# Kernel tuning notes

Measured on AMD Instinct MI355X. Metric: run time of the kernel, lower is better.

Reference implementation:

```python
import jax, jax.numpy as jnp
import numpy as np

B, S, C, HEADS, EXP = 8, 1024, 256, 8, 4
H = W = 32  # S = H*W
HID = EXP * C
RATES = (1, 6, 12, 18)
EPS = 1e-5


def _conv(x, w, b=None, dilation=1, padding=0):
    out = jax.lax.conv_general_dilated(
        x, w, (1, 1), [(padding, padding), (padding, padding)],
        rhs_dilation=(dilation, dilation),
        dimension_numbers=('NCHW', 'OIHW', 'NCHW'))
    if b is not None:
        out = out + b[None, :, None, None]
    return out


def _bn(x, g, b, m, v):
    # inference-mode BatchNorm2d
    s = (g / jnp.sqrt(v + EPS))[None, :, None, None]
    return (x - m[None, :, None, None]) * s + b[None, :, None, None]


def _ln(x, g, b):
    mu = jnp.mean(x, -1, keepdims=True)
    var = jnp.mean((x - mu) ** 2, -1, keepdims=True)
    return (x - mu) / jnp.sqrt(var + EPS) * g + b


def setup_inputs() -> dict:
    key = jax.random.key(0)
    ks = iter(jax.random.split(key, 64))

    def n(shape, s=0.05):
        return jax.random.normal(next(ks), shape, jnp.float32) * s

    def u(shape):
        return jax.random.uniform(next(ks), shape, jnp.float32, 0.5, 1.5)

    inp = {
        'value': n((B, S, C), 1.0),
        'key': n((B, S, C), 1.0),
        'query': n((B, S, C), 1.0),
        'res': n((B, S, C), 1.0),
        # nn.MultiheadAttention params
        'attn_wi': n((3 * C, C)), 'attn_bi': jnp.zeros((3 * C,)),
        'attn_wo': n((C, C)), 'attn_bo': jnp.zeros((C,)),
        # Modulator params
        'mod_bias': jnp.zeros((1, C, 1, 1)),
        'ca_w1': n((C // 16, C)), 'ca_w2': n((C, C // 16)),
        'pa_w': n((C, C, 1, 1)),
        'pa_bn_g': jnp.ones((C,)), 'pa_bn_b': jnp.zeros((C,)),
        'pa_bn_m': n((C,), 0.1), 'pa_bn_v': u((C,)),
        'sa_w': n((4, C, C, 3, 3)), 'sa_b': jnp.zeros((4, C)),
        'sa_bn_g': jnp.ones((4, C)), 'sa_bn_b': jnp.zeros((4, C)),
        'sa_bn_m': n((4, C), 0.1), 'sa_bn_v': u((4, C)),
        'sa_out_w': n((C, 4 * C, 1, 1)), 'sa_out_b': jnp.zeros((C,)),
        'out_w': n((C, C, 1, 1)), 'out_b': jnp.zeros((C,)),
        'out_bn_g': jnp.ones((C,)), 'out_bn_b': jnp.zeros((C,)),
        'out_bn_m': n((C,), 0.1), 'out_bn_v': u((C,)),
        # LayerNorms
        'ln1_g': jnp.ones((C,)), 'ln1_b': jnp.zeros((C,)),
        'ln2_g': jnp.ones((C,)), 'ln2_b': jnp.zeros((C,)),
        # E_MLP params
        'mlp_w1': n((HID, C)), 'mlp_b1': jnp.zeros((HID,)),
        'dw_w': n((HID, HID, 3, 3), 0.02), 'dw_b': jnp.zeros((HID,)),
        'pw_w': n((HID, HID, 3, 3), 0.02), 'pw_b': jnp.zeros((HID,)),
        'mlp_w2': n((C, HID)), 'mlp_b2': jnp.zeros((C,)),
    }
    return inp


def reference(value, key, query, res,
              attn_wi, attn_bi, attn_wo, attn_bo,
              mod_bias, ca_w1, ca_w2, pa_w,
              pa_bn_g, pa_bn_b, pa_bn_m, pa_bn_v,
              sa_w, sa_b, sa_bn_g, sa_bn_b, sa_bn_m, sa_bn_v,
              sa_out_w, sa_out_b, out_w, out_b,
              out_bn_g, out_bn_b, out_bn_m, out_bn_v,
              ln1_g, ln1_b, ln2_g, ln2_b,
              mlp_w1, mlp_b1, dw_w, dw_b, pw_w, pw_b, mlp_w2, mlp_b2):
    d = C // HEADS
    # SMA arg shuffle: block calls sma(query,key,value) -> SMA(value=query,key=key,query=value)
    # -> nn.MultiheadAttention(query=value_blk, key=key_blk, value=query_blk)
    q = (value @ attn_wi[:C].T + attn_bi[:C]).reshape(B, S, HEADS, d)
    k = (key @ attn_wi[C:2 * C].T + attn_bi[C:2 * C]).reshape(B, S, HEADS, d)
    v = (query @ attn_wi[2 * C:].T + attn_bi[2 * C:]).reshape(B, S, HEADS, d)
    scores = jnp.einsum('bqhd,bkhd->bhqk', q, k) / jnp.sqrt(jnp.float32(d))
    attn = jax.nn.softmax(scores, axis=-1)
    ctx = jnp.einsum('bhqk,bkhd->bqhd', attn, v).reshape(B, S, C)
    msa = ctx @ attn_wo.T + attn_bo                       # [B,S,C]

    x = msa.transpose(0, 2, 1).reshape(B, C, H, W)        # [B,C,H,W]

    # --- Modulator ---
    pa = x * jax.nn.sigmoid(_bn(_conv(x, pa_w), pa_bn_g, pa_bn_b, pa_bn_m, pa_bn_v))
    y = jnp.mean(x, axis=(2, 3))                          # [B,C]
    y = jax.nn.sigmoid(jax.nn.relu(y @ ca_w1.T) @ ca_w2.T)
    ca = x * y[:, :, None, None]
    pa_ca = jax.nn.softmax(pa @ ca, axis=-1)              # [B,C,H,H] (H==W)
    sa_outs = [_bn(jax.nn.relu(_conv(x, sa_w[i], sa_b[i], dilation=r, padding=r)),
                   sa_bn_g[i], sa_bn_b[i], sa_bn_m[i], sa_bn_v[i])
               for i, r in enumerate(RATES)]
    sa = _conv(jnp.concatenate(sa_outs, axis=1), sa_out_w, sa_out_b)
    out = pa_ca @ sa                                      # [B,C,H,W]
    out = _bn(_conv(out, out_w, out_b), out_bn_g, out_bn_b, out_bn_m, out_bn_v)
    syn = out + mod_bias + x                              # residual inside modulator

    attn_seq = syn.reshape(B, C, S).transpose(0, 2, 1)    # [B,S,C]
    q2 = _ln(attn_seq + res, ln1_g, ln1_b)

    # --- E_MLP ---
    h = jax.nn.gelu(q2 @ mlp_w1.T + mlp_b1, approximate=False)  # [B,S,4C]
    hc = h.transpose(0, 2, 1).reshape(B, HID, H, W)
    hc = _conv(hc, dw_w, dw_b, padding=1)
    hc = _conv(hc, pw_w, pw_b, padding=1)
    h2 = hc.reshape(B, HID, S).transpose(0, 2, 1)
    ff = h2 @ mlp_w2.T + mlp_b2
    return _ln(ff + q2, ln2_g, ln2_b)
```

## Files before the change

### kernel.cpp

```cpp
#include <hip/hip_runtime.h>
#include <hip/hip_bf16.h>
#include <math.h>

typedef __attribute__((ext_vector_type(8))) short bf16x8;
typedef __attribute__((ext_vector_type(4))) short bf16x4;
typedef __attribute__((ext_vector_type(4))) float f32x4;

#define MM 8192
#define CC 256

__device__ __forceinline__ short f2bf(float f) {
  unsigned u = __float_as_uint(f);
  u = (u + 0x7FFFu + ((u >> 16) & 1u)) >> 16;
  return (short)u;
}

__device__ __forceinline__ void gload16(const short* g, short* l) {
  __builtin_amdgcn_global_load_lds(
      (const __attribute__((address_space(1))) unsigned int*)(g),
      (__attribute__((address_space(3))) unsigned int*)(l), 16, 0, 0);
}

__global__ __launch_bounds__(256, 2) void convh_k(const short* __restrict__ Ain,
                                                  const short* __restrict__ Wt,
                                                  short* __restrict__ outB,
                                                  const float* __restrict__ bias) {
  extern __shared__ short sm[];
  const int tid = threadIdx.x;
  const int bx = blockIdx.x;
  const int bm = bx & 63, bn = bx >> 6;
  const int l = tid & 63, w = tid >> 6;
  const int wm = w >> 1, wn = w & 1;
  const int lr = l & 15, lg = l >> 4;
  const int lsub = l >> 3;
  const int srcu = (l & 7) ^ lsub;
  const int img = bm >> 3, rbase = (bm & 7) * 4;
  const bf16x8 zv = {0, 0, 0, 0, 0, 0, 0, 0};

  f32x4 acc[4][4];
#pragma unroll
  for (int i = 0; i < 4; ++i)
#pragma unroll
    for (int j = 0; j < 4; ++j) acc[i][j] = (f32x4){0.f, 0.f, 0.f, 0.f};

  const short* wsrc[4];
#pragma unroll
  for (int i = 0; i < 4; ++i) {
    int rowi = (w * 4 + i) * 8 + lsub;
    wsrc[i] = Wt + (size_t)(bn * 128 + rowi) * 1024 + srcu * 8;
  }

  const short* asrc[6]; int apos[6]; bool avalid[6];
#pragma unroll
  for (int i = 0; i < 6; ++i) {
    int ug = tid + i * 256;
    int pos = ug >> 3, u = ug & 7;
    int irow = pos >> 5, px = pos & 31;
    int grow = rbase + irow - 1;
    avalid[i] = ((unsigned)grow < 32u);
    int growc = grow < 0 ? 0 : (grow > 31 ? 31 : grow);
    asrc[i] = Ain + ((size_t)(img * 1024 + growc * 32 + px)) * 1024 + u * 8;
    apos[i] = pos * 64 + ((u ^ (pos & 7)) << 3);
  }

  bf16x8 areg[6];
  auto issueA = [&](int kc) {
#pragma unroll
    for (int i = 0; i < 6; ++i)
      areg[i] = *(const bf16x8*)(asrc[i] + kc * 64);
  };
  auto writeA = [&](int ab) {
    short* abuf = sm + 16384 + ab * 12288;
#pragma unroll
    for (int i = 0; i < 6; ++i)
      *(bf16x8*)(abuf + apos[i]) = avalid[i] ? areg[i] : zv;
  };
  auto issueW = [&](int kc, int tap, int wb) {
    short* base = sm + wb * 8192;
    size_t wo = (size_t)tap * 1048576 + (size_t)kc * 64;
#pragma unroll
    for (int i = 0; i < 4; ++i)
      gload16(wsrc[i] + wo, base + (w * 4 + i) * 512);
  };
  auto compute = [&](int dy, int dx, const short* bA, const short* bB) {
    __builtin_amdgcn_s_setprio(1);
#pragma unroll
    for (int ks = 0; ks < 64; ks += 32) {
      const int u = (ks >> 3) + lg;
      bf16x8 af[4], bfr[4];
#pragma unroll
      for (int mt = 0; mt < 4; ++mt) {
        int px = (mt & 1) * 16 + lr;
        int ipx = px + dx;
        bool okx = ((unsigned)ipx < 32u);
        int pos = (wm * 2 + (mt >> 1) + 1 + dy) * 32 + (ipx & 31);
        bf16x8 v = *(const bf16x8*)&bA[pos * 64 + ((u ^ (pos & 7)) << 3)];
        af[mt] = okx ? v : zv;
      }
#pragma unroll
      for (int nt = 0; nt < 4; ++nt)
        bfr[nt] = *(const bf16x8*)&bB[(wn * 64 + nt * 16 + lr) * 64 + ((u ^ (lr & 7)) << 3)];
#pragma unroll
      for (int mt = 0; mt < 4; ++mt)
#pragma unroll
        for (int nt = 0; nt < 4; ++nt)
          acc[mt][nt] = __builtin_amdgcn_mfma_f32_16x16x32_bf16(af[mt], bfr[nt], acc[mt][nt], 0, 0, 0);
    }
    __builtin_amdgcn_s_setprio(0);
  };

  issueA(0);
  issueW(0, 0, 0);
  issueW(0, 1, 1);
  asm volatile("s_waitcnt vmcnt(4)" ::: "memory");
  writeA(0);
  asm volatile("s_waitcnt lgkmcnt(0)" ::: "memory");

  for (int kc = 0; kc < 16; ++kc) {
    const int ab = kc & 1;
    const short* bA = sm + 16384 + ab * 12288;
#pragma unroll
    for (int tap = 0; tap < 9; ++tap) {
      const int wb = (kc + tap) & 1;
      const short* bB = sm + wb * 8192;
      if (tap == 7) {
        if (kc < 15) asm volatile("s_waitcnt vmcnt(10)" ::: "memory");
        else         asm volatile("s_waitcnt vmcnt(4)" ::: "memory");
      } else if (tap == 8) {
        if (kc < 15) asm volatile("s_waitcnt vmcnt(4)" ::: "memory");
        else         asm volatile("s_waitcnt vmcnt(0)" ::: "memory");
      } else {
        asm volatile("s_waitcnt vmcnt(4)" ::: "memory");
      }
      asm volatile("s_barrier" ::: "memory");
      compute(tap / 3 - 1, tap % 3 - 1, bA, bB);
      asm volatile("s_barrier" ::: "memory");
      if (tap <= 6) {
        if (tap == 6 && kc < 15) issueA(kc + 1);
        issueW(kc, tap + 2, wb);
      } else if (tap == 7) {
        if (kc < 15) issueW(kc + 1, 0, wb);
      } else {
        if (kc < 15) {
          writeA(ab ^ 1);
          asm volatile("s_waitcnt lgkmcnt(0)" ::: "memory");
          issueW(kc + 1, 1, wb);
        }
      }
    }
  }

#pragma unroll
  for (int nt = 0; nt < 4; ++nt) {
    const int col = bn * 128 + wn * 64 + nt * 16 + lr;
    const float bi = bias[col];
#pragma unroll
    for (int mt = 0; mt < 4; ++mt) {
      const int row0 = bm * 128 + wm * 64 + mt * 16 + lg * 4;
#pragma unroll
      for (int j = 0; j < 4; ++j)
        outB[(size_t)(row0 + j) * 1024 + col] = f2bf(acc[mt][nt][j] + bi);
    }
  }
}

struct GP {
  const short* A; const short* W; float* outF; short* outB; float* outT;
  const float* bias; const float* scale; const float* shift; const float* aux;
  const short* zero;
  long aZStride, wZStride, oZStride;
  int N, Kc, ldA, ldOut, outColOff, outZOff;
  int dil0, dil1, dil2, dil3;
  int T, nkcs;
};

template<int TAPS, int EPI, int OUTMODE, int TSTORE>
__global__ __launch_bounds__(256, 2) void gemmd_k(GP p) {
  extern __shared__ short sm[];
  const int tid = threadIdx.x;
  const int bx = blockIdx.x, bz = blockIdx.z;
  const int bm = bx & 63, bn = bx >> 6;
  const int l = tid & 63, w = tid >> 6;
  const int wm = w >> 1, wn = w & 1;
  const int lr = l & 15, lg = l >> 4;
  const int lsub = l >> 3;
  const int srcu = (l & 7) ^ lsub;

  const short* Abase = p.A + (size_t)bz * p.aZStride;
  const short* Wbase = p.W + (size_t)bz * p.wZStride;
  const int dil = (TAPS == 9)
      ? (bz == 0 ? p.dil0 : bz == 1 ? p.dil1 : bz == 2 ? p.dil2 : p.dil3) : 1;

  f32x4 acc[4][4];
#pragma unroll
  for (int i = 0; i < 4; ++i)
#pragma unroll
    for (int j = 0; j < 4; ++j) acc[i][j] = (f32x4){0.f, 0.f, 0.f, 0.f};

  int rowi[4], prow[4], bimg[4], py[4], px[4];
  const short* wsrc[4];
#pragma unroll
  for (int i = 0; i < 4; ++i) {
    rowi[i] = (w * 4 + i) * 8 + lsub;
    prow[i] = bm * 128 + rowi[i];
    bimg[i] = prow[i] >> 10; py[i] = (prow[i] >> 5) & 31; px[i] = prow[i] & 31;
    wsrc[i] = Wbase + (size_t)(bn * 128 + rowi[i]) * p.Kc + srcu * 8;
  }
  const size_t wTap = (size_t)p.N * p.Kc;
  const int nkcMask = (1 << p.nkcs) - 1;

  auto issue = [&](int t, int buf) {
    const int tap = t >> p.nkcs;
    const int kc = t & nkcMask;
    short* base = sm + buf * 16384;
    if (TAPS == 1) {
#pragma unroll
      for (int i = 0; i < 4; ++i)
        gload16(Abase + (size_t)prow[i] * p.ldA + kc * 64 + srcu * 8,
                base + (w * 4 + i) * 512);
    } else {
      const int dy = (tap / 3 - 1) * dil, dx = (tap % 3 - 1) * dil;
#pragma unroll
      for (int i = 0; i < 4; ++i) {
        int yy = py[i] + dy, xx = px[i] + dx;
        bool ok = ((unsigned)yy < 32u) & ((unsigned)xx < 32u);
        const short* a = ok
            ? Abase + (size_t)((bimg[i] << 10) + (yy << 5) + xx) * p.ldA + kc * 64
            : p.zero;
        gload16(a + srcu * 8, base + (w * 4 + i) * 512);
      }
    }
    short* bbase = base + 8192;
    const size_t wo = (size_t)tap * wTap + kc * 64;
#pragma unroll
    for (int i = 0; i < 4; ++i)
      gload16(wsrc[i] + wo, bbase + (w * 4 + i) * 512);
  };

  auto compute = [&](int buf) {
    const short* bA = sm + buf * 16384;
    const short* bB = bA + 8192;
    __builtin_amdgcn_s_setprio(1);
#pragma unroll
    for (int ks = 0; ks < 64; ks += 32) {
      const int u = (ks >> 3) + lg;
      bf16x8 af[4], bfr[4];
#pragma unroll
      for (int mt = 0; mt < 4; ++mt)
        af[mt] = *(bf16x8*)&bA[(wm * 64 + mt * 16 + lr) * 64 + ((u ^ (lr & 7)) << 3)];
#pragma unroll
      for (int nt = 0; nt < 4; ++nt)
        bfr[nt] = *(bf16x8*)&bB[(wn * 64 + nt * 16 + lr) * 64 + ((u ^ (lr & 7)) << 3)];
#pragma unroll
      for (int mt = 0; mt < 4; ++mt)
#pragma unroll
        for (int nt = 0; nt < 4; ++nt)
          acc[mt][nt] = __builtin_amdgcn_mfma_f32_16x16x32_bf16(af[mt], bfr[nt], acc[mt][nt], 0, 0, 0);
    }
    __builtin_amdgcn_s_setprio(0);
  };

  issue(0, 0);
  if (p.T > 1) issue(1, 1);
  int cur = 0;
  for (int t = 0; t < p.T; ++t) {
    if (t + 1 < p.T) asm volatile("s_waitcnt vmcnt(8)" ::: "memory");
    else             asm volatile("s_waitcnt vmcnt(0)" ::: "memory");
    asm volatile("s_barrier" ::: "memory");
    compute(cur);
    asm volatile("s_barrier" ::: "memory");
    if (t + 2 < p.T) issue(t + 2, cur);
    cur ^= 1;
  }

  float* outF = p.outF + (size_t)bz * p.oZStride;
  short* outB = p.outB + (size_t)bz * p.oZStride;
#pragma unroll
  for (int nt = 0; nt < 4; ++nt) {
    const int col = bn * 128 + wn * 64 + nt * 16 + lr;
    const int gcol = p.outColOff + bz * p.outZOff + col;
    const float bi = (p.bias != nullptr) ? p.bias[bz * p.N + col] : 0.f;
    float scl = 0.f, shf = 0.f;
    if (EPI == 3 || EPI == 4 || EPI == 5) {
      scl = p.scale[bz * p.N + col]; shf = p.shift[bz * p.N + col];
    }
#pragma unroll
    for (int mt = 0; mt < 4; ++mt) {
      const int row0 = bm * 128 + wm * 64 + mt * 16 + lg * 4;
      f32x4 vv;
#pragma unroll
      for (int j = 0; j < 4; ++j) {
        const long row = row0 + j;
        float v = acc[mt][nt][j];
        if (EPI == 1 || EPI == 2 || EPI == 3) v += bi;
        if (EPI == 2) v = 0.5f * v * (1.f + erff(v * 0.70710678118654752f));
        if (EPI == 3) { v = fmaxf(v, 0.f); v = v * scl + shf; }
        if (EPI == 4) {
          float t2 = v * scl + shf;
          float sg = 1.f / (1.f + __expf(-t2));
          v = p.aux[row * 256 + col] * sg;
        }
        if (EPI == 5) v = v * scl + shf + p.aux[row * 256 + col];
        vv[j] = v;
        if (OUTMODE == 0 || OUTMODE == 2) outF[row * (long)p.ldOut + gcol] = v;
        if (OUTMODE == 1 || OUTMODE == 2) outB[row * (long)p.ldOut + gcol] = f2bf(v);
      }
      if (TSTORE) {
        float* t = p.outT + ((size_t)(row0 >> 10) * 256 + gcol) * 1024 + (row0 & 1023);
        *(f32x4*)t = vv;
      }
    }
  }
}

__global__ __launch_bounds__(256) void attn_k(const short* qb, const short* kb,
                                              const short* vb, short* ctx) {
  __shared__ short lK[128 * 40];
  __shared__ short lVt[32 * 136];
  __shared__ short lP[4][16 * 136];
  const int tid = threadIdx.x;
  const int qt = blockIdx.x;
  const int bh = blockIdx.y;
  const int b = bh >> 3, h = bh & 7;
  const int l = tid & 63, wv = tid >> 6;
  const int lr = l & 15, lg = l >> 4;
  const float SC = 0.17677669529663687f;

  const int qrow = qt * 64 + wv * 16 + lr;
  const bf16x8 qf = *(const bf16x8*)(qb + ((size_t)(b * 1024 + qrow)) * 256 + h * 32 + lg * 8);

  f32x4 o0 = {0.f,0.f,0.f,0.f}, o1 = {0.f,0.f,0.f,0.f};
  float m[4] = {-1e30f, -1e30f, -1e30f, -1e30f};
  float lsum[4] = {0.f, 0.f, 0.f, 0.f};

  for (int ch = 0; ch < 8; ++ch) {
    __syncthreads();
    {
      const int keyi = tid >> 1, d0 = (tid & 1) * 16;
      const short* src = kb + ((size_t)(b * 1024 + ch * 128 + keyi)) * 256 + h * 32 + d0;
      short* dst = &lK[keyi * 40 + d0];
      *(bf16x8*)dst = *(const bf16x8*)src;
      *(bf16x8*)(dst + 8) = *(const bf16x8*)(src + 8);
    }
    {
      const int keyi = tid >> 1, d0 = (tid & 1) * 16;
      const short* src = vb + ((size_t)(b * 1024 + ch * 128 + keyi)) * 256 + h * 32 + d0;
      short tmp[16];
      *(bf16x8*)tmp = *(const bf16x8*)src;
      *(bf16x8*)(tmp + 8) = *(const bf16x8*)(src + 8);
#pragma unroll
      for (int j = 0; j < 16; ++j) lVt[(d0 + j) * 136 + keyi] = tmp[j];
    }
    __syncthreads();

    f32x4 sc[8];
#pragma unroll
    for (int jt = 0; jt < 8; ++jt) {
      bf16x8 bfr = *(bf16x8*)&lK[(jt * 16 + lr) * 40 + lg * 8];
      sc[jt] = __builtin_amdgcn_mfma_f32_16x16x32_bf16(qf, bfr, (f32x4){0.f,0.f,0.f,0.f}, 0, 0, 0);
      sc[jt] *= SC;
    }
#pragma unroll
    for (int j = 0; j < 4; ++j) {
      float rm = -1e30f;
#pragma unroll
      for (int jt = 0; jt < 8; ++jt) rm = fmaxf(rm, sc[jt][j]);
      rm = fmaxf(rm, __shfl_xor(rm, 1));
      rm = fmaxf(rm, __shfl_xor(rm, 2));
      rm = fmaxf(rm, __shfl_xor(rm, 4));
      rm = fmaxf(rm, __shfl_xor(rm, 8));
      float mn = fmaxf(m[j], rm);
      float alpha = exp2f((m[j] - mn) * 1.44269504088896f);
      m[j] = mn;
      float rs = 0.f;
#pragma unroll
      for (int jt = 0; jt < 8; ++jt) {
        float pv = exp2f((sc[jt][j] - mn) * 1.44269504088896f);
        sc[jt][j] = pv;
        rs += pv;
      }
      rs += __shfl_xor(rs, 1); rs += __shfl_xor(rs, 2);
      rs += __shfl_xor(rs, 4); rs += __shfl_xor(rs, 8);
      lsum[j] = lsum[j] * alpha + rs;
      o0[j] *= alpha; o1[j] *= alpha;
      const int prw = lg * 4 + j;
#pragma unroll
      for (int jt = 0; jt < 8; ++jt) lP[wv][prw * 136 + jt * 16 + lr] = f2bf(sc[jt][j]);
    }
#pragma unroll
    for (int kc = 0; kc < 4; ++kc) {
      bf16x8 pf = *(bf16x8*)&lP[wv][lr * 136 + kc * 32 + lg * 8];
      bf16x8 v0 = *(bf16x8*)&lVt[lr * 136 + kc * 32 + lg * 8];
      bf16x8 v1 = *(bf16x8*)&lVt[(16 + lr) * 136 + kc * 32 + lg * 8];
      o0 = __builtin_amdgcn_mfma_f32_16x16x32_bf16(pf, v0, o0, 0, 0, 0);
      o1 = __builtin_amdgcn_mfma_f32_16x16x32_bf16(pf, v1, o1, 0, 0, 0);
    }
  }
  const size_t orow = (size_t)(b * 1024 + qt * 64 + wv * 16);
#pragma unroll
  for (int j = 0; j < 4; ++j) {
    float inv = 1.f / lsum[j];
    ctx[(orow + lg * 4 + j) * 256 + h * 32 + lr]      = f2bf(o0[j] * inv);
    ctx[(orow + lg * 4 + j) * 256 + h * 32 + 16 + lr] = f2bf(o1[j] * inv);
  }
}

__global__ __launch_bounds__(256) void cvt4_k(const float* src, short* dst, int n4) {
  int i = blockIdx.x * 256 + threadIdx.x;
  if (i < n4) {
    f32x4 v = ((const f32x4*)src)[i];
    bf16x4 o;
    o[0] = f2bf(v[0]); o[1] = f2bf(v[1]); o[2] = f2bf(v[2]); o[3] = f2bf(v[3]);
    ((bf16x4*)dst)[i] = o;
  }
}

__global__ __launch_bounds__(256) void zero_k(short* p) {
  p[blockIdx.x * 256 + threadIdx.x] = 0;
}

__global__ __launch_bounds__(256) void tap_k(const float* src, short* dst, int n) {
  int i = blockIdx.x * 256 + threadIdx.x;
  if (i >= n) return;
  const float* s = src + (size_t)i * 9;
  float v[9];
#pragma unroll
  for (int t = 0; t < 9; ++t) v[t] = s[t];
#pragma unroll
  for (int t = 0; t < 9; ++t) dst[(size_t)t * n + i] = f2bf(v[t]);
}

__global__ void bnprep_k(const float* pg, const float* pb, const float* pm, const float* pv,
                         const float* sg, const float* sb, const float* sm, const float* sv,
                         const float* og, const float* ob, const float* om, const float* ov,
                         const float* conv_ob, const float* mbias, float* out) {
  int c = threadIdx.x;
  float s = pg[c] / sqrtf(pv[c] + 1e-5f);
  out[c] = s;
  out[256 + c] = pb[c] - pm[c] * s;
  for (int i = 0; i < 4; ++i) {
    int idx = i * 256 + c;
    float ss = sg[idx] / sqrtf(sv[idx] + 1e-5f);
    out[512 + idx] = ss;
    out[1536 + idx] = sb[idx] - sm[idx] * ss;
  }
  float os = og[c] / sqrtf(ov[c] + 1e-5f);
  out[2560 + c] = os;
  out[2816 + c] = ob[c] - om[c] * os + conv_ob[c] * os + mbias[c];
}

__global__ __launch_bounds__(256) void tposeb_k(const float* src, short* dst) {
  __shared__ float tile[32][33];
  int pc = blockIdx.x, cc = blockIdx.y, b = blockIdx.z;
  int tx = threadIdx.x & 31, ty = threadIdx.x >> 5;
  const float* s = src + ((size_t)b * 256 + cc * 32) * 1024 + pc * 32;
#pragma unroll
  for (int k = 0; k < 4; ++k)
    tile[ty + 8 * k][tx] = s[(ty + 8 * k) * 1024 + tx];
  __syncthreads();
  short* d = dst + ((size_t)b * 1024 + pc * 32) * 256 + cc * 32;
#pragma unroll
  for (int k = 0; k < 4; ++k)
    d[(ty + 8 * k) * 256 + tx] = f2bf(tile[tx][ty + 8 * k]);
}

__global__ __launch_bounds__(256) void camean_k(const float* x, float* partial) {
  int blk = blockIdx.x, c = threadIdx.x;
  const float* px = x + ((size_t)blk * 64) * 256 + c;
  float s = 0.f;
#pragma unroll 4
  for (int r = 0; r < 64; ++r) s += px[(size_t)r * 256];
  partial[blk * 256 + c] = s;
}

__global__ __launch_bounds__(256) void ca2_k(const float* partial, const float* w1,
                                             const float* w2, float* y2) {
  __shared__ float ly[256];
  __shared__ float ly1[16];
  int b = blockIdx.x, c = threadIdx.x;
  float s = 0.f;
#pragma unroll
  for (int j = 0; j < 16; ++j) s += partial[(b * 16 + j) * 256 + c];
  ly[c] = s * (1.f / 1024.f);
  __syncthreads();
  if (c < 16) {
    float a = 0.f;
    const float* wp = w1 + c * 256;
    for (int i = 0; i < 256; ++i) a += ly[i] * wp[i];
    ly1[c] = fmaxf(a, 0.f);
  }
  __syncthreads();
  float a = 0.f;
  const float* wp = w2 + c * 16;
#pragma unroll
  for (int j = 0; j < 16; ++j) a += ly1[j] * wp[j];
  y2[b * 256 + c] = 1.f / (1.f + __expf(-a));
}

__global__ __launch_bounds__(256) void bm1_k(const float* paT, const float* xT,
                                             const float* y2, float* pa_ca) {
  __shared__ float sp[32][33], sx[32][33], so[32][33];
  __shared__ float rinv[32];
  int bc = blockIdx.x, t = threadIdx.x;
  for (int e = t; e < 1024; e += 256) {
    sp[e >> 5][e & 31] = paT[(size_t)bc * 1024 + e];
    sx[e >> 5][e & 31] = xT[(size_t)bc * 1024 + e];
  }
  __syncthreads();
  float yv = y2[bc];
  int i = t >> 3, j0 = (t & 7) * 4;
  float a0 = 0.f, a1 = 0.f, a2 = 0.f, a3 = 0.f;
  for (int k = 0; k < 32; ++k) {
    float pv = sp[i][k];
    a0 += pv * sx[k][j0];     a1 += pv * sx[k][j0 + 1];
    a2 += pv * sx[k][j0 + 2]; a3 += pv * sx[k][j0 + 3];
  }
  so[i][j0] = a0 * yv; so[i][j0 + 1] = a1 * yv;
  so[i][j0 + 2] = a2 * yv; so[i][j0 + 3] = a3 * yv;
  __syncthreads();
  if (t < 32) {
    float mx = -1e30f;
    for (int j = 0; j < 32; ++j) mx = fmaxf(mx, so[t][j]);
    float sum = 0.f;
    for (int j = 0; j < 32; ++j) { float pp = __expf(so[t][j] - mx); so[t][j] = pp; sum += pp; }
    rinv[t] = 1.f / sum;
  }
  __syncthreads();
  for (int e = t; e < 1024; e += 256)
    pa_ca[(size_t)bc * 1024 + e] = so[e >> 5][e & 31] * rinv[e >> 5];
}

__global__ __launch_bounds__(256) void bm2_k(const float* pa_ca, const float* saT, float* moT) {
  __shared__ float sp[32][33], ss[32][33];
  int bc = blockIdx.x, t = threadIdx.x;
  for (int e = t; e < 1024; e += 256) {
    sp[e >> 5][e & 31] = pa_ca[(size_t)bc * 1024 + e];
    ss[e >> 5][e & 31] = saT[(size_t)bc * 1024 + e];
  }
  __syncthreads();
  int i = t >> 3, j0 = (t & 7) * 4;
  float a0 = 0.f, a1 = 0.f, a2 = 0.f, a3 = 0.f;
  for (int k = 0; k < 32; ++k) {
    float pv = sp[i][k];
    a0 += pv * ss[k][j0];     a1 += pv * ss[k][j0 + 1];
    a2 += pv * ss[k][j0 + 2]; a3 += pv * ss[k][j0 + 3];
  }
  size_t base = (size_t)bc * 1024 + i * 32 + j0;
  moT[base] = a0; moT[base + 1] = a1; moT[base + 2] = a2; moT[base + 3] = a3;
}

template<int DUAL>
__global__ __launch_bounds__(256) void ln_k(const float* in, const float* res,
                                            const float* g, const float* bta,
                                            float* out, short* outB) {
  __shared__ float red[8];
  size_t row = blockIdx.x;
  int c = threadIdx.x;
  int wv = c >> 6, lane = c & 63;
  float v = in[row * 256 + c] + res[row * 256 + c];
  float s = v;
  for (int mk = 1; mk < 64; mk <<= 1) s += __shfl_xor(s, mk);
  if (lane == 0) red[wv] = s;
  __syncthreads();
  float mu = (red[0] + red[1] + red[2] + red[3]) * (1.f / 256.f);
  float d = v - mu;
  float q = d * d;
  for (int mk = 1; mk < 64; mk <<= 1) q += __shfl_xor(q, mk);
  if (lane == 0) red[4 + wv] = q;
  __syncthreads();
  float var = (red[4] + red[5] + red[6] + red[7]) * (1.f / 256.f);
  float o = d * rsqrtf(var + 1e-5f) * g[c] + bta[c];
  out[row * 256 + c] = o;
  if (DUAL) outB[row * 256 + c] = f2bf(o);
}

extern "C" void kernel_launch(void* const* d_in, const int* in_sizes, int n_in,
                              void* d_out, int out_size, void* d_ws, size_t ws_size,
                              hipStream_t stream) {
  (void)in_sizes; (void)n_in; (void)out_size; (void)ws_size;
  const float* value    = (const float*)d_in[0];
  const float* key      = (const float*)d_in[1];
  const float* query    = (const float*)d_in[2];
  const float* res      = (const float*)d_in[3];
  const float* attn_wi  = (const float*)d_in[4];
  const float* attn_bi  = (const float*)d_in[5];
  const float* attn_wo  = (const float*)d_in[6];
  const float* attn_bo  = (const float*)d_in[7];
  const float* mod_bias = (const float*)d_in[8];
  const float* ca_w1    = (const float*)d_in[9];
  const float* ca_w2    = (const float*)d_in[10];
  const float* pa_w     = (const float*)d_in[11];
  const float* pa_bn_g  = (const float*)d_in[12];
  const float* pa_bn_b  = (const float*)d_in[13];
  const float* pa_bn_m  = (const float*)d_in[14];
  const float* pa_bn_v  = (const float*)d_in[15];
  const float* sa_w     = (const float*)d_in[16];
  const float* sa_b     = (const float*)d_in[17];
  const float* sa_bn_g  = (const float*)d_in[18];
  const float* sa_bn_b  = (const float*)d_in[19];
  const float* sa_bn_m  = (const float*)d_in[20];
  const float* sa_bn_v  = (const float*)d_in[21];
  const float* sa_out_w = (const float*)d_in[22];
  const float* sa_out_b = (const float*)d_in[23];
  const float* out_w    = (const float*)d_in[24];
  const float* out_b    = (const float*)d_in[25];
  const float* out_bn_g = (const float*)d_in[26];
  const float* out_bn_b = (const float*)d_in[27];
  const float* out_bn_m = (const float*)d_in[28];
  const float* out_bn_v = (const float*)d_in[29];
  const float* ln1_g    = (const float*)d_in[30];
  const float* ln1_b    = (const float*)d_in[31];
  const float* ln2_g    = (const float*)d_in[32];
  const float* ln2_b    = (const float*)d_in[33];
  const float* mlp_w1   = (const float*)d_in[34];
  const float* mlp_b1   = (const float*)d_in[35];
  const float* dw_w     = (const float*)d_in[36];
  const float* dw_b     = (const float*)d_in[37];
  const float* pw_w     = (const float*)d_in[38];
  const float* pw_b     = (const float*)d_in[39];
  const float* mlp_w2   = (const float*)d_in[40];
  const float* mlp_b2   = (const float*)d_in[41];

  char* ws = (char*)d_ws;
  const size_t MB = 1024 * 1024;
  char* A = ws + 0 * MB;
  char* Bx = ws + 16 * MB;
  char* Cx = ws + 32 * MB;
  float* xbuf  = (float*)(ws + 40 * MB);
  short* xbf   = (short*)(ws + 48 * MB);
  char* Fx = ws + 52 * MB;
  float* q2buf = (float*)(ws + 60 * MB);
  short* q2B   = (short*)(ws + 68 * MB);
  short* wdw   = (short*)(ws + 72 * MB);
  short* wpw   = (short*)(ws + 90 * MB);
  size_t o = 108 * MB;
  short* w_awi  = (short*)(ws + o); o += 768 * 256 * 2;
  short* w_awo  = (short*)(ws + o); o += 256 * 256 * 2;
  short* w_pa   = (short*)(ws + o); o += 256 * 256 * 2;
  short* w_sa   = (short*)(ws + o); o += (size_t)4 * 9 * 256 * 256 * 2;
  short* w_saou = (short*)(ws + o); o += 256 * 1024 * 2;
  short* w_out  = (short*)(ws + o); o += 256 * 256 * 2;
  short* w_mlp1 = (short*)(ws + o); o += 1024 * 256 * 2;
  short* w_mlp2 = (short*)(ws + o); o += 256 * 1024 * 2;
  float* bn     = (float*)(ws + o); o += 3072 * 4;
  float* y2buf  = (float*)(ws + o); o += 8 * 256 * 4;
  float* capart = (float*)(ws + o); o += 128 * 256 * 4;
  short* zbuf   = (short*)(ws + o); o += 2048 * 2;

  short* vkq  = (short*)A;
  short* qkv  = (short*)Bx;
  short* ctxB = (short*)Cx;
  float* xT   = (float*)A;
  float* paT  = (float*)(A + 8 * MB);
  float* pa_ca = (float*)Bx;
  short* saCat = (short*)A;
  float* saT  = (float*)Cx;
  float* moT  = (float*)Fx;
  short* modB = (short*)Cx;
  float* synBuf = (float*)Fx;
  short* hB   = (short*)A;
  short* hc1B = (short*)Bx;
  short* h2B  = (short*)A;
  float* ffBuf = (float*)Cx;

  const int LDSB = 2 * 16384 * 2;
  const int LDSC = 40960 * 2;
  hipFuncSetAttribute((const void*)gemmd_k<1, 1, 1, 0>, hipFuncAttributeMaxDynamicSharedMemorySize, LDSB);
  hipFuncSetAttribute((const void*)gemmd_k<1, 1, 2, 1>, hipFuncAttributeMaxDynamicSharedMemorySize, LDSB);
  hipFuncSetAttribute((const void*)gemmd_k<1, 4, 3, 1>, hipFuncAttributeMaxDynamicSharedMemorySize, LDSB);
  hipFuncSetAttribute((const void*)gemmd_k<9, 3, 1, 0>, hipFuncAttributeMaxDynamicSharedMemorySize, LDSB);
  hipFuncSetAttribute((const void*)gemmd_k<1, 1, 3, 1>, hipFuncAttributeMaxDynamicSharedMemorySize, LDSB);
  hipFuncSetAttribute((const void*)gemmd_k<1, 5, 0, 0>, hipFuncAttributeMaxDynamicSharedMemorySize, LDSB);
  hipFuncSetAttribute((const void*)gemmd_k<1, 2, 1, 0>, hipFuncAttributeMaxDynamicSharedMemorySize, LDSB);
  hipFuncSetAttribute((const void*)gemmd_k<1, 1, 0, 0>, hipFuncAttributeMaxDynamicSharedMemorySize, LDSB);
  hipFuncSetAttribute((const void*)convh_k, hipFuncAttributeMaxDynamicSharedMemorySize, LDSC);

  zero_k<<<8, 256, 0, stream>>>(zbuf);
  cvt4_k<<<192, 256, 0, stream>>>(attn_wi, w_awi, 768 * 64);
  cvt4_k<<<64, 256, 0, stream>>>(attn_wo, w_awo, 256 * 64);
  cvt4_k<<<64, 256, 0, stream>>>(pa_w, w_pa, 256 * 64);
  for (int i4 = 0; i4 < 4; ++i4)
    tap_k<<<256, 256, 0, stream>>>(sa_w + (size_t)i4 * 589824,
                                   w_sa + (size_t)i4 * 589824, 65536);
  cvt4_k<<<256, 256, 0, stream>>>(sa_out_w, w_saou, 1024 * 64);
  cvt4_k<<<64, 256, 0, stream>>>(out_w, w_out, 256 * 64);
  cvt4_k<<<256, 256, 0, stream>>>(mlp_w1, w_mlp1, 1024 * 64);
  cvt4_k<<<256, 256, 0, stream>>>(mlp_w2, w_mlp2, 1024 * 64);
  tap_k<<<4096, 256, 0, stream>>>(dw_w, wdw, 1048576);
  tap_k<<<4096, 256, 0, stream>>>(pw_w, wpw, 1048576);
  bnprep_k<<<1, 256, 0, stream>>>(pa_bn_g, pa_bn_b, pa_bn_m, pa_bn_v,
                                  sa_bn_g, sa_bn_b, sa_bn_m, sa_bn_v,
                                  out_bn_g, out_bn_b, out_bn_m, out_bn_v,
                                  out_b, mod_bias, bn);
  cvt4_k<<<2048, 256, 0, stream>>>(value, vkq, MM * 64);
  cvt4_k<<<2048, 256, 0, stream>>>(key,   vkq + (size_t)MM * 256, MM * 64);
  cvt4_k<<<2048, 256, 0, stream>>>(query, vkq + (size_t)2 * MM * 256, MM * 64);

  GP g;
  g.zero = zbuf; g.scale = nullptr; g.shift = nullptr; g.aux = nullptr;
  g.aZStride = 0; g.wZStride = 0; g.oZStride = 0;
  g.outColOff = 0; g.outZOff = 0;
  g.dil0 = 1; g.dil1 = 1; g.dil2 = 1; g.dil3 = 1;
  g.outF = nullptr; g.outB = nullptr; g.outT = nullptr;

  g.A = vkq; g.W = w_awi; g.outB = qkv; g.bias = attn_bi;
  g.N = 256; g.Kc = 256; g.ldA = 256; g.ldOut = 256; g.T = 4; g.nkcs = 2;
  g.aZStride = (size_t)MM * 256; g.wZStride = 256 * 256; g.oZStride = (size_t)MM * 256;
  gemmd_k<1, 1, 1, 0><<<dim3(128, 1, 3), 256, LDSB, stream>>>(g);
  g.aZStride = 0; g.wZStride = 0; g.oZStride = 0;

  attn_k<<<dim3(16, 64), 256, 0, stream>>>(qkv, qkv + (size_t)MM * 256,
                                           qkv + (size_t)2 * MM * 256, ctxB);

  g.A = ctxB; g.W = w_awo; g.outF = xbuf; g.outB = xbf; g.outT = xT; g.bias = attn_bo;
  gemmd_k<1, 1, 2, 1><<<dim3(128), 256, LDSB, stream>>>(g);

  g.A = xbf; g.W = w_pa; g.outF = nullptr; g.outB = nullptr; g.outT = paT; g.bias = nullptr;
  g.scale = bn; g.shift = bn + 256; g.aux = xbuf;
  gemmd_k<1, 4, 3, 1><<<dim3(128), 256, LDSB, stream>>>(g);
  g.scale = nullptr; g.shift = nullptr; g.aux = nullptr;

  camean_k<<<128, 256, 0, stream>>>(xbuf, capart);
  ca2_k<<<8, 256, 0, stream>>>(capart, ca_w1, ca_w2, y2buf);
  bm1_k<<<2048, 256, 0, stream>>>(paT, xT, y2buf, pa_ca);

  g.A = xbf; g.W = w_sa; g.outB = saCat; g.outF = nullptr; g.outT = nullptr;
  g.bias = sa_b; g.scale = bn + 512; g.shift = bn + 1536;
  g.ldOut = 1024; g.outZOff = 256; g.wZStride = (size_t)9 * 256 * 256;
  g.dil0 = 1; g.dil1 = 6; g.dil2 = 12; g.dil3 = 18;
  g.T = 36; g.nkcs = 2;
  gemmd_k<9, 3, 1, 0><<<dim3(128, 1, 4), 256, LDSB, stream>>>(g);
  g.outZOff = 0; g.wZStride = 0; g.scale = nullptr; g.shift = nullptr;
  g.dil0 = 1; g.dil1 = 1; g.dil2 = 1; g.dil3 = 1;

  g.A = saCat; g.W = w_saou; g.outB = nullptr; g.outT = saT; g.bias = sa_out_b;
  g.N = 256; g.Kc = 1024; g.ldA = 1024; g.ldOut = 256; g.T = 16; g.nkcs = 4;
  gemmd_k<1, 1, 3, 1><<<dim3(128), 256, LDSB, stream>>>(g);

  bm2_k<<<2048, 256, 0, stream>>>(pa_ca, saT, moT);
  tposeb_k<<<dim3(32, 8, 8), 256, 0, stream>>>(moT, modB);

  g.A = modB; g.W = w_out; g.outF = synBuf; g.outT = nullptr; g.bias = nullptr;
  g.scale = bn + 2560; g.shift = bn + 2816; g.aux = xbuf;
  g.N = 256; g.Kc = 256; g.ldA = 256; g.ldOut = 256; g.T = 4; g.nkcs = 2;
  gemmd_k<1, 5, 0, 0><<<dim3(128), 256, LDSB, stream>>>(g);
  g.scale = nullptr; g.shift = nullptr; g.aux = nullptr;

  ln_k<1><<<8192, 256, 0, stream>>>(synBuf, res, ln1_g, ln1_b, q2buf, q2B);

  g.A = q2B; g.W = w_mlp1; g.outB = hB; g.outF = nullptr; g.bias = mlp_b1;
  g.N = 1024; g.Kc = 256; g.ldA = 256; g.ldOut = 1024; g.T = 4; g.nkcs = 2;
  gemmd_k<1, 2, 1, 0><<<dim3(512), 256, LDSB, stream>>>(g);

  convh_k<<<dim3(512), 256, LDSC, stream>>>(hB, wdw, hc1B, dw_b);

  convh_k<<<dim3(512), 256, LDSC, stream>>>(hc1B, wpw, h2B, pw_b);

  g.A = h2B; g.W = w_mlp2; g.outF = ffBuf; g.outB = nullptr; g.bias = mlp_b2;
  g.N = 256; g.Kc = 1024; g.ldA = 1024; g.ldOut = 256; g.T = 16; g.nkcs = 4;
  gemmd_k<1, 1, 0, 0><<<dim3(128), 256, LDSB, stream>>>(g);

  ln_k<0><<<8192, 256, 0, stream>>>(ffBuf, q2buf, ln2_g, ln2_b, (float*)d_out, nullptr);
}
```

Before: 563.2 us.

## Add half-size 64x64 GEMM tile variant for N=256 GEMMs to fill more CUs

Adds a HALF template parameter to the GEMM kernel that uses 64x64 block tiles instead of 128x128. The N=256 GEMMs now launch 512 blocks instead of 128. The intent is to fill all CUs on the MI355X, which 128 blocks leave underused. The convh kernel's block-index mapping is also reordered so that adjacent blocks share M rows. In exchange, the smaller tiles reuse less data per block and do fewer MFMAs per LDS load.

```diff
diff --git a/kernel.cpp b/kernel.cpp
--- a/kernel.cpp
+++ b/kernel.cpp
@@ -28,7 +28,7 @@
   extern __shared__ short sm[];
   const int tid = threadIdx.x;
   const int bx = blockIdx.x;
-  const int bm = bx & 63, bn = bx >> 6;
+  const int bm = bx >> 3, bn = bx & 7;
   const int l = tid & 63, w = tid >> 6;
   const int wm = w >> 1, wn = w & 1;
   const int lr = l & 15, lg = l >> 4;
@@ -174,12 +174,21 @@
   int T, nkcs;
 };
 
-template<int TAPS, int EPI, int OUTMODE, int TSTORE>
+template<int TAPS, int EPI, int OUTMODE, int TSTORE, int HALF>
 __global__ __launch_bounds__(256, 2) void gemmd_k(GP p) {
   extern __shared__ short sm[];
+  constexpr int RG   = HALF ? 2 : 4;
+  constexpr int MT   = HALF ? 2 : 4;
+  constexpr int NT   = HALF ? 2 : 4;
+  constexpr int WTs  = HALF ? 32 : 64;
+  constexpr int BMr  = HALF ? 64 : 128;
+  constexpr int BNr  = HALF ? 64 : 128;
+  constexpr int BSTR = HALF ? 8192 : 16384;
+  constexpr int BOFF = HALF ? 4096 : 8192;
   const int tid = threadIdx.x;
   const int bx = blockIdx.x, bz = blockIdx.z;
-  const int bm = bx & 63, bn = bx >> 6;
+  const int bm = HALF ? (bx >> 2) : (bx & 63);
+  const int bn = HALF ? (bx & 3) : (bx >> 6);
   const int l = tid & 63, w = tid >> 6;
   const int wm = w >> 1, wn = w & 1;
   const int lr = l & 15, lg = l >> 4;
@@ -191,20 +200,20 @@
   const int dil = (TAPS == 9)
       ? (bz == 0 ? p.dil0 : bz == 1 ? p.dil1 : bz == 2 ? p.dil2 : p.dil3) : 1;
 
-  f32x4 acc[4][4];
-#pragma unroll
-  for (int i = 0; i < 4; ++i)
-#pragma unroll
-    for (int j = 0; j < 4; ++j) acc[i][j] = (f32x4){0.f, 0.f, 0.f, 0.f};
-
-  int rowi[4], prow[4], bimg[4], py[4], px[4];
-  const short* wsrc[4];
-#pragma unroll
-  for (int i = 0; i < 4; ++i) {
-    rowi[i] = (w * 4 + i) * 8 + lsub;
-    prow[i] = bm * 128 + rowi[i];
+  f32x4 acc[MT][NT];
+#pragma unroll
+  for (int i = 0; i < MT; ++i)
+#pragma unroll
+    for (int j = 0; j < NT; ++j) acc[i][j] = (f32x4){0.f, 0.f, 0.f, 0.f};
+
+  int rowi[RG], prow[RG], bimg[RG], py[RG], px[RG];
+  const short* wsrc[RG];
+#pragma unroll
+  for (int i = 0; i < RG; ++i) {
+    rowi[i] = (w * RG + i) * 8 + lsub;
+    prow[i] = bm * BMr + rowi[i];
     bimg[i] = prow[i] >> 10; py[i] = (prow[i] >> 5) & 31; px[i] = prow[i] & 31;
-    wsrc[i] = Wbase + (size_t)(bn * 128 + rowi[i]) * p.Kc + srcu * 8;
+    wsrc[i] = Wbase + (size_t)(bn * BNr + rowi[i]) * p.Kc + srcu * 8;
   }
   const size_t wTap = (size_t)p.N * p.Kc;
   const int nkcMask = (1 << p.nkcs) - 1;
@@ -212,49 +221,49 @@
   auto issue = [&](int t, int buf) {
     const int tap = t >> p.nkcs;
     const int kc = t & nkcMask;
-    short* base = sm + buf * 16384;
+    short* base = sm + buf * BSTR;
     if (TAPS == 1) {
 #pragma unroll
-      for (int i = 0; i < 4; ++i)
+      for (int i = 0; i < RG; ++i)
         gload16(Abase + (size_t)prow[i] * p.ldA + kc * 64 + srcu * 8,
-                base + (w * 4 + i) * 512);
+                base + (w * RG + i) * 512);
     } else {
       const int dy = (tap / 3 - 1) * dil, dx = (tap % 3 - 1) * dil;
 #pragma unroll
-      for (int i = 0; i < 4; ++i) {
+      for (int i = 0; i < RG; ++i) {
         int yy = py[i] + dy, xx = px[i] + dx;
         bool ok = ((unsigned)yy < 32u) & ((unsigned)xx < 32u);
         const short* a = ok
             ? Abase + (size_t)((bimg[i] << 10) + (yy << 5) + xx) * p.ldA + kc * 64
             : p.zero;
-        gload16(a + srcu * 8, base + (w * 4 + i) * 512);
+        gload16(a + srcu * 8, base + (w * RG + i) * 512);
       }
     }
-    short* bbase = base + 8192;
+    short* bbase = base + BOFF;
     const size_t wo = (size_t)tap * wTap + kc * 64;
 #pragma unroll
-    for (int i = 0; i < 4; ++i)
-      gload16(wsrc[i] + wo, bbase + (w * 4 + i) * 512);
+    for (int i = 0; i < RG; ++i)
+      gload16(wsrc[i] + wo, bbase + (w * RG + i) * 512);
   };
 
   auto compute = [&](int buf) {
-    const short* bA = sm + buf * 16384;
-    const short* bB = bA + 8192;
+    const short* bA = sm + buf * BSTR;
+    const short* bB = bA + BOFF;
     __builtin_amdgcn_s_setprio(1);
 #pragma unroll
     for (int ks = 0; ks < 64; ks += 32) {
       const int u = (ks >> 3) + lg;
-      bf16x8 af[4], bfr[4];
-#pragma unroll
-      for (int mt = 0; mt < 4; ++mt)
-        af[mt] = *(bf16x8*)&bA[(wm * 64 + mt * 16 + lr) * 64 + ((u ^ (lr & 7)) << 3)];
-#pragma unroll
-      for (int nt = 0; nt < 4; ++nt)
-        bfr[nt] = *(bf16x8*)&bB[(wn * 64 + nt * 16 + lr) * 64 + ((u ^ (lr & 7)) << 3)];
-#pragma unroll
-      for (int mt = 0; mt < 4; ++mt)
-#pragma unroll
-        for (int nt = 0; nt < 4; ++nt)
+      bf16x8 af[MT], bfr[NT];
+#pragma unroll
+      for (int mt = 0; mt < MT; ++mt)
+        af[mt] = *(bf16x8*)&bA[(wm * WTs + mt * 16 + lr) * 64 + ((u ^ (lr & 7)) << 3)];
+#pragma unroll
+      for (int nt = 0; nt < NT; ++nt)
+        bfr[nt] = *(bf16x8*)&bB[(wn * WTs + nt * 16 + lr) * 64 + ((u ^ (lr & 7)) << 3)];
+#pragma unroll
+      for (int mt = 0; mt < MT; ++mt)
+#pragma unroll
+        for (int nt = 0; nt < NT; ++nt)
           acc[mt][nt] = __builtin_amdgcn_mfma_f32_16x16x32_bf16(af[mt], bfr[nt], acc[mt][nt], 0, 0, 0);
     }
     __builtin_amdgcn_s_setprio(0);
@@ -264,8 +273,12 @@
   if (p.T > 1) issue(1, 1);
   int cur = 0;
   for (int t = 0; t < p.T; ++t) {
-    if (t + 1 < p.T) asm volatile("s_waitcnt vmcnt(8)" ::: "memory");
-    else             asm volatile("s_waitcnt vmcnt(0)" ::: "memory");
+    if (t + 1 < p.T) {
+      if (HALF) asm volatile("s_waitcnt vmcnt(4)" ::: "memory");
+      else      asm volatile("s_waitcnt vmcnt(8)" ::: "memory");
+    } else {
+      asm volatile("s_waitcnt vmcnt(0)" ::: "memory");
+    }
     asm volatile("s_barrier" ::: "memory");
     compute(cur);
     asm volatile("s_barrier" ::: "memory");
@@ -276,8 +289,8 @@
   float* outF = p.outF + (size_t)bz * p.oZStride;
   short* outB = p.outB + (size_t)bz * p.oZStride;
 #pragma unroll
-  for (int nt = 0; nt < 4; ++nt) {
-    const int col = bn * 128 + wn * 64 + nt * 16 + lr;
+  for (int nt = 0; nt < NT; ++nt) {
+    const int col = bn * BNr + wn * WTs + nt * 16 + lr;
     const int gcol = p.outColOff + bz * p.outZOff + col;
     const float bi = (p.bias != nullptr) ? p.bias[bz * p.N + col] : 0.f;
     float scl = 0.f, shf = 0.f;
@@ -285,8 +298,8 @@
       scl = p.scale[bz * p.N + col]; shf = p.shift[bz * p.N + col];
     }
 #pragma unroll
-    for (int mt = 0; mt < 4; ++mt) {
-      const int row0 = bm * 128 + wm * 64 + mt * 16 + lg * 4;
+    for (int mt = 0; mt < MT; ++mt) {
+      const int row0 = bm * BMr + wm * WTs + mt * 16 + lg * 4;
       f32x4 vv;
 #pragma unroll
       for (int j = 0; j < 4; ++j) {
@@ -664,15 +677,16 @@
   float* ffBuf = (float*)Cx;
 
   const int LDSB = 2 * 16384 * 2;
+  const int LDSH = 2 * 8192 * 2;
   const int LDSC = 40960 * 2;
-  hipFuncSetAttribute((const void*)gemmd_k<1, 1, 1, 0>, hipFuncAttributeMaxDynamicSharedMemorySize, LDSB);
-  hipFuncSetAttribute((const void*)gemmd_k<1, 1, 2, 1>, hipFuncAttributeMaxDynamicSharedMemorySize, LDSB);
-  hipFuncSetAttribute((const void*)gemmd_k<1, 4, 3, 1>, hipFuncAttributeMaxDynamicSharedMemorySize, LDSB);
-  hipFuncSetAttribute((const void*)gemmd_k<9, 3, 1, 0>, hipFuncAttributeMaxDynamicSharedMemorySize, LDSB);
-  hipFuncSetAttribute((const void*)gemmd_k<1, 1, 3, 1>, hipFuncAttributeMaxDynamicSharedMemorySize, LDSB);
-  hipFuncSetAttribute((const void*)gemmd_k<1, 5, 0, 0>, hipFuncAttributeMaxDynamicSharedMemorySize, LDSB);
-  hipFuncSetAttribute((const void*)gemmd_k<1, 2, 1, 0>, hipFuncAttributeMaxDynamicSharedMemorySize, LDSB);
-  hipFuncSetAttribute((const void*)gemmd_k<1, 1, 0, 0>, hipFuncAttributeMaxDynamicSharedMemorySize, LDSB);
+  hipFuncSetAttribute((const void*)gemmd_k<1, 1, 1, 0, 1>, hipFuncAttributeMaxDynamicSharedMemorySize, LDSH);
+  hipFuncSetAttribute((const void*)gemmd_k<1, 1, 2, 1, 1>, hipFuncAttributeMaxDynamicSharedMemorySize, LDSH);
+  hipFuncSetAttribute((const void*)gemmd_k<1, 4, 3, 1, 1>, hipFuncAttributeMaxDynamicSharedMemorySize, LDSH);
+  hipFuncSetAttribute((const void*)gemmd_k<9, 3, 1, 0, 0>, hipFuncAttributeMaxDynamicSharedMemorySize, LDSB);
+  hipFuncSetAttribute((const void*)gemmd_k<1, 1, 3, 1, 1>, hipFuncAttributeMaxDynamicSharedMemorySize, LDSH);
+  hipFuncSetAttribute((const void*)gemmd_k<1, 5, 0, 0, 1>, hipFuncAttributeMaxDynamicSharedMemorySize, LDSH);
+  hipFuncSetAttribute((const void*)gemmd_k<1, 2, 1, 0, 0>, hipFuncAttributeMaxDynamicSharedMemorySize, LDSB);
+  hipFuncSetAttribute((const void*)gemmd_k<1, 1, 0, 0, 1>, hipFuncAttributeMaxDynamicSharedMemorySize, LDSH);
   hipFuncSetAttribute((const void*)convh_k, hipFuncAttributeMaxDynamicSharedMemorySize, LDSC);
 
   zero_k<<<8, 256, 0, stream>>>(zbuf);
@@ -706,18 +720,18 @@
   g.A = vkq; g.W = w_awi; g.outB = qkv; g.bias = attn_bi;
   g.N = 256; g.Kc = 256; g.ldA = 256; g.ldOut = 256; g.T = 4; g.nkcs = 2;
   g.aZStride = (size_t)MM * 256; g.wZStride = 256 * 256; g.oZStride = (size_t)MM * 256;
-  gemmd_k<1, 1, 1, 0><<<dim3(128, 1, 3), 256, LDSB, stream>>>(g);
+  gemmd_k<1, 1, 1, 0, 1><<<dim3(512, 1, 3), 256, LDSH, stream>>>(g);
   g.aZStride = 0; g.wZStride = 0; g.oZStride = 0;
 
   attn_k<<<dim3(16, 64), 256, 0, stream>>>(qkv, qkv + (size_t)MM * 256,
                                            qkv + (size_t)2 * MM * 256, ctxB);
 
   g.A = ctxB; g.W = w_awo; g.outF = xbuf; g.outB = xbf; g.outT = xT; g.bias = attn_bo;
-  gemmd_k<1, 1, 2, 1><<<dim3(128), 256, LDSB, stream>>>(g);
+  gemmd_k<1, 1, 2, 1, 1><<<dim3(512), 256, LDSH, stream>>>(g);
 
   g.A = xbf; g.W = w_pa; g.outF = nullptr; g.outB = nullptr; g.outT = paT; g.bias = nullptr;
   g.scale = bn; g.shift = bn + 256; g.aux = xbuf;
-  gemmd_k<1, 4, 3, 1><<<dim3(128), 256, LDSB, stream>>>(g);
+  gemmd_k<1, 4, 3, 1, 1><<<dim3(512), 256, LDSH, stream>>>(g);
   g.scale = nullptr; g.shift = nullptr; g.aux = nullptr;
 
   camean_k<<<128, 256, 0, stream>>>(xbuf, capart);
@@ -729,13 +743,13 @@
   g.ldOut = 1024; g.outZOff = 256; g.wZStride = (size_t)9 * 256 * 256;
   g.dil0 = 1; g.dil1 = 6; g.dil2 = 12; g.dil3 = 18;
   g.T = 36; g.nkcs = 2;
-  gemmd_k<9, 3, 1, 0><<<dim3(128, 1, 4), 256, LDSB, stream>>>(g);
+  gemmd_k<9, 3, 1, 0, 0><<<dim3(128, 1, 4), 256, LDSB, stream>>>(g);
   g.outZOff = 0; g.wZStride = 0; g.scale = nullptr; g.shift = nullptr;
   g.dil0 = 1; g.dil1 = 1; g.dil2 = 1; g.dil3 = 1;
 
   g.A = saCat; g.W = w_saou; g.outB = nullptr; g.outT = saT; g.bias = sa_out_b;
   g.N = 256; g.Kc = 1024; g.ldA = 1024; g.ldOut = 256; g.T = 16; g.nkcs = 4;
-  gemmd_k<1, 1, 3, 1><<<dim3(128), 256, LDSB, stream>>>(g);
+  gemmd_k<1, 1, 3, 1, 1><<<dim3(512), 256, LDSH, stream>>>(g);
 
   bm2_k<<<2048, 256, 0, stream>>>(pa_ca, saT, moT);
   tposeb_k<<<dim3(32, 8, 8), 256, 0, stream>>>(moT, modB);
@@ -743,14 +757,14 @@
   g.A = modB; g.W = w_out; g.outF = synBuf; g.outT = nullptr; g.bias = nullptr;
   g.scale = bn + 2560; g.shift = bn + 2816; g.aux = xbuf;
   g.N = 256; g.Kc = 256; g.ldA = 256; g.ldOut = 256; g.T = 4; g.nkcs = 2;
-  gemmd_k<1, 5, 0, 0><<<dim3(128), 256, LDSB, stream>>>(g);
+  gemmd_k<1, 5, 0, 0, 1><<<dim3(512), 256, LDSH, stream>>>(g);
   g.scale = nullptr; g.shift = nullptr; g.aux = nullptr;
 
   ln_k<1><<<8192, 256, 0, stream>>>(synBuf, res, ln1_g, ln1_b, q2buf, q2B);
 
   g.A = q2B; g.W = w_mlp1; g.outB = hB; g.outF = nullptr; g.bias = mlp_b1;
   g.N = 1024; g.Kc = 256; g.ldA = 256; g.ldOut = 1024; g.T = 4; g.nkcs = 2;
-  gemmd_k<1, 2, 1, 0><<<dim3(512), 256, LDSB, stream>>>(g);
+  gemmd_k<1, 2, 1, 0, 0><<<dim3(512), 256, LDSB, stream>>>(g);
 
   convh_k<<<dim3(512), 256, LDSC, stream>>>(hB, wdw, hc1B, dw_b);
 
@@ -758,7 +772,7 @@
 
   g.A = h2B; g.W = w_mlp2; g.outF = ffBuf; g.outB = nullptr; g.bias = mlp_b2;
   g.N = 256; g.Kc = 1024; g.ldA = 1024; g.ldOut = 256; g.T = 16; g.nkcs = 4;
-  gemmd_k<1, 1, 0, 0><<<dim3(128), 256, LDSB, stream>>>(g);
+  gemmd_k<1, 1, 0, 0, 1><<<dim3(512), 256, LDSH, stream>>>(g);
 
   ln_k<0><<<8192, 256, 0, stream>>>(ffBuf, q2buf, ln2_g, ln2_b, (float*)d_out, nullptr);
 }
```

Measured after the change: 540.9 us. -4.0%, faster.
